# Performance work log

Hardware: AMD Instinct MI355X
Metric: run time of the kernel (lower is better)

Reference implementation:

```python
import jax, jax.numpy as jnp
import numpy as np

N, D = 16384, 2048

def setup_inputs() -> dict:
    key = jax.random.key(0)
    k1, k2, k3 = jax.random.split(key, 3)
    x1 = jax.random.normal(k1, (N, D), dtype=jnp.float32)
    x2 = jax.random.normal(k2, (N, D), dtype=jnp.float32)
    w = jax.random.normal(k3, (D,), dtype=jnp.float32)
    return {"x1": x1, "x2": x2, "w": w}

def reference(x1, x2, w):
    # per-row attention scores: s_k[i] = dot(x_k[i], w)
    s1 = x1 @ w  # [N]
    s2 = x2 @ w  # [N]
    # alpha_1 = exp(s1)/(exp(s1)+exp(s2)) == sigmoid(s1 - s2) (numerically stable)
    alpha1 = jax.nn.sigmoid(s1 - s2)  # [N]
    alpha2 = 1.0 - alpha1
    fused = alpha1[:, None] * x1 + alpha2[:, None] * x2  # [N, D]
    alpha = jnp.stack([alpha1, alpha2], axis=1)  # [N, 2], detached in original
    return fused, alpha
```

## Files before the change

### kernel.cpp

```cpp
#include <hip/hip_runtime.h>


#define NROWS 16384
#define DCOLS 2048
#define NF4 ((size_t)NROWS * (DCOLS / 4))

typedef float f32x4 __attribute__((ext_vector_type(4)));
typedef float f32x2 __attribute__((ext_vector_type(2)));

__global__ __launch_bounds__(256) void dot_kernel(
    const float* __restrict__ x1,
    const float* __restrict__ x2,
    const float* __restrict__ w,
    float* __restrict__ alpha)
{
    const int lane = threadIdx.x & 63;
    const size_t row = (size_t)(blockIdx.x << 2) + (threadIdx.x >> 6);

    const f32x4* __restrict__ x1v = (const f32x4*)(x1 + row * DCOLS);
    const f32x4* __restrict__ x2v = (const f32x4*)(x2 + row * DCOLS);
    const f32x4* __restrict__ wv  = (const f32x4*)w;

    float p = 0.0f;
    #pragma unroll
    for (int i = 0; i < 8; ++i) {
        const f32x4 a  = x1v[lane + (i << 6)];
        const f32x4 b  = x2v[lane + (i << 6)];
        const f32x4 ww = wv[lane + (i << 6)];
        p = fmaf(a.x - b.x, ww.x, p);
        p = fmaf(a.y - b.y, ww.y, p);
        p = fmaf(a.z - b.z, ww.z, p);
        p = fmaf(a.w - b.w, ww.w, p);
    }

    #pragma unroll
    for (int off = 32; off > 0; off >>= 1)
        p += __shfl_down(p, off, 64);

    if (lane == 0) {
        const float g = 1.0f / (1.0f + expf(-p));
        f32x2 al;
        al.x = g;
        al.y = 1.0f - g;
        *(f32x2*)(alpha + row * 2) = al;
    }
}

__global__ __launch_bounds__(256) void fuse_kernel(
    const float* __restrict__ x1,
    const float* __restrict__ x2,
    const float* __restrict__ alpha,
    float* __restrict__ fused)
{
    const f32x4* __restrict__ av = (const f32x4*)x1;
    const f32x4* __restrict__ bv = (const f32x4*)x2;
    f32x4* __restrict__ ov = (f32x4*)fused;

    const size_t stride = (size_t)gridDim.x * 256;
    size_t i = (size_t)blockIdx.x * 256 + threadIdx.x;

    #pragma unroll 4
    for (; i < NF4; i += stride) {
        const float g = alpha[(i >> 9) << 1];
        const f32x4 a = av[i];
        const f32x4 b = bv[i];
        f32x4 f;
        f.x = fmaf(g, a.x - b.x, b.x);
        f.y = fmaf(g, a.y - b.y, b.y);
        f.z = fmaf(g, a.z - b.z, b.z);
        f.w = fmaf(g, a.w - b.w, b.w);
        __builtin_nontemporal_store(f, ov + i);
    }
}

extern "C" void kernel_launch(void* const* d_in, const int* in_sizes, int n_in,
                              void* d_out, int out_size, void* d_ws, size_t ws_size,
                              hipStream_t stream)
{
    const float* x1 = (const float*)d_in[0];
    const float* x2 = (const float*)d_in[1];
    const float* w  = (const float*)d_in[2];

    float* fused = (float*)d_out;
    float* alpha = fused + (size_t)NROWS * DCOLS;

    dot_kernel<<<NROWS / 4, 256, 0, stream>>>(x1, x2, w, alpha);
    fuse_kernel<<<2048, 256, 0, stream>>>(x1, x2, alpha, fused);
}
```

Baseline: 357.6 us.

## Split row dot product into separate x1 and x2 passes, two rows per wave

```diff
diff --git a/kernel.cpp b/kernel.cpp
--- a/kernel.cpp
+++ b/kernel.cpp
@@ -8,41 +8,77 @@
 typedef float f32x4 __attribute__((ext_vector_type(4)));
 typedef float f32x2 __attribute__((ext_vector_type(2)));
 
-__global__ __launch_bounds__(256) void dot_kernel(
-    const float* __restrict__ x1,
-    const float* __restrict__ x2,
+__global__ __launch_bounds__(256) void dot_x1_kernel(
+    const float* __restrict__ x,
     const float* __restrict__ w,
+    float* __restrict__ s)
+{
+    const int lane = threadIdx.x & 63;
+    const size_t r0 = ((size_t)blockIdx.x * 4 + (threadIdx.x >> 6)) * 2;
+
+    const f32x4* __restrict__ xv = (const f32x4*)(x + r0 * DCOLS);
+    const f32x4* __restrict__ wv = (const f32x4*)w;
+
+    float pa = 0.0f, pb = 0.0f;
+    #pragma unroll
+    for (int i = 0; i < 8; ++i) {
+        const f32x4 xa = xv[lane + (i << 6)];
+        const f32x4 xb = xv[lane + ((i + 8) << 6)];
+        const f32x4 ww = wv[lane + (i << 6)];
+        pa = fmaf(xa.x, ww.x, pa); pa = fmaf(xa.y, ww.y, pa);
+        pa = fmaf(xa.z, ww.z, pa); pa = fmaf(xa.w, ww.w, pa);
+        pb = fmaf(xb.x, ww.x, pb); pb = fmaf(xb.y, ww.y, pb);
+        pb = fmaf(xb.z, ww.z, pb); pb = fmaf(xb.w, ww.w, pb);
+    }
+
+    #pragma unroll
+    for (int off = 32; off > 0; off >>= 1) {
+        pa += __shfl_down(pa, off, 64);
+        pb += __shfl_down(pb, off, 64);
+    }
+
+    if (lane == 0) {
+        f32x2 sv; sv.x = pa; sv.y = pb;
+        *(f32x2*)(s + r0) = sv;
+    }
+}
+
+__global__ __launch_bounds__(256) void dot_x2_kernel(
+    const float* __restrict__ x,
+    const float* __restrict__ w,
+    const float* __restrict__ s1,
     float* __restrict__ alpha)
 {
     const int lane = threadIdx.x & 63;
-    const size_t row = (size_t)(blockIdx.x << 2) + (threadIdx.x >> 6);
+    const size_t r0 = ((size_t)blockIdx.x * 4 + (threadIdx.x >> 6)) * 2;
 
-    const f32x4* __restrict__ x1v = (const f32x4*)(x1 + row * DCOLS);
-    const f32x4* __restrict__ x2v = (const f32x4*)(x2 + row * DCOLS);
-    const f32x4* __restrict__ wv  = (const f32x4*)w;
+    const f32x4* __restrict__ xv = (const f32x4*)(x + r0 * DCOLS);
+    const f32x4* __restrict__ wv = (const f32x4*)w;
 
-    float p = 0.0f;
+    float pa = 0.0f, pb = 0.0f;
     #pragma unroll
     for (int i = 0; i < 8; ++i) {
-        const f32x4 a  = x1v[lane + (i << 6)];
-        const f32x4 b  = x2v[lane + (i << 6)];
+        const f32x4 xa = xv[lane + (i << 6)];
+        const f32x4 xb = xv[lane + ((i + 8) << 6)];
         const f32x4 ww = wv[lane + (i << 6)];
-        p = fmaf(a.x - b.x, ww.x, p);
-        p = fmaf(a.y - b.y, ww.y, p);
-        p = fmaf(a.z - b.z, ww.z, p);
-        p = fmaf(a.w - b.w, ww.w, p);
+        pa = fmaf(xa.x, ww.x, pa); pa = fmaf(xa.y, ww.y, pa);
+        pa = fmaf(xa.z, ww.z, pa); pa = fmaf(xa.w, ww.w, pa);
+        pb = fmaf(xb.x, ww.x, pb); pb = fmaf(xb.y, ww.y, pb);
+        pb = fmaf(xb.z, ww.z, pb); pb = fmaf(xb.w, ww.w, pb);
     }
 
     #pragma unroll
-    for (int off = 32; off > 0; off >>= 1)
-        p += __shfl_down(p, off, 64);
+    for (int off = 32; off > 0; off >>= 1) {
+        pa += __shfl_down(pa, off, 64);
+        pb += __shfl_down(pb, off, 64);
+    }
 
     if (lane == 0) {
-        const float g = 1.0f / (1.0f + expf(-p));
-        f32x2 al;
-        al.x = g;
-        al.y = 1.0f - g;
-        *(f32x2*)(alpha + row * 2) = al;
+        const f32x2 s1v = *(const f32x2*)(s1 + r0);
+        const float ga = 1.0f / (1.0f + expf(-(s1v.x - pa)));
+        const float gb = 1.0f / (1.0f + expf(-(s1v.y - pb)));
+        f32x4 al; al.x = ga; al.y = 1.0f - ga; al.z = gb; al.w = 1.0f - gb;
+        *(f32x4*)(alpha + r0 * 2) = al;
     }
 }
 
@@ -83,7 +119,9 @@
 
     float* fused = (float*)d_out;
     float* alpha = fused + (size_t)NROWS * DCOLS;
+    float* s1    = (float*)d_ws;
 
-    dot_kernel<<<NROWS / 4, 256, 0, stream>>>(x1, x2, w, alpha);
+    dot_x1_kernel<<<2048, 256, 0, stream>>>(x1, w, s1);
+    dot_x2_kernel<<<2048, 256, 0, stream>>>(x2, w, s1, alpha);
     fuse_kernel<<<2048, 256, 0, stream>>>(x1, x2, alpha, fused);
 }
```

Result: no change. 356.3 us (-0.4%).
